# Optimization experiments

Measured on AMD Instinct MI355X. Metric: run time of the kernel, lower is better.

Reference implementation:

```python
import jax, jax.numpy as jnp
import numpy as np
import math

DIM, SCALES, ORIENTS, K = 32, 3, 8, 15
SIGMA, GAMMA = 5.0, 0.5
B, H, W = 4, 128, 128

def _make_gabor_filters():
    # matches EnhancedBlockGabor._create_complex_filters
    coords = np.arange(-(K // 2), K // 2 + 1, dtype=np.float32)
    y, x = np.meshgrid(coords, coords, indexing='ij')  # torch.meshgrid default 'ij'
    filts = []
    for s in range(SCALES):
        fu = 1.0 / 2 ** s
        for o in range(ORIENTS):
            theta = o * math.pi / ORIENTS
            xt = x * math.cos(theta) + y * math.sin(theta)
            yt = -x * math.sin(theta) + y * math.cos(theta)
            env = np.exp(-(xt ** 2 + GAMMA ** 2 * yt ** 2) / (2 * SIGMA ** 2))
            amp = fu ** 2 / (math.pi * GAMMA ** 2)
            real = amp * env * np.cos(2 * math.pi * fu * xt)
            imag = amp * env * np.sin(2 * math.pi * fu * xt)
            filts.append(np.stack([real, imag]))
    return jnp.asarray(np.stack(filts), dtype=jnp.float32)  # (S*O, 2, K, K)

def setup_inputs() -> dict:
    key = jax.random.key(0)
    k1, k2, k3 = jax.random.split(key, 3)
    x = jax.random.normal(k1, (B, DIM, H, W), dtype=jnp.float32)
    filters = _make_gabor_filters()
    cin = DIM * SCALES * ORIENTS
    w1 = jax.random.normal(k2, (DIM, cin), dtype=jnp.float32) / np.sqrt(cin)
    b1 = jax.random.normal(k3, (DIM,), dtype=jnp.float32) * 0.01
    return {"x": x, "filters": filters, "w1": w1, "b1": b1}

def reference(x, filters, w1, b1):
    Bb, C, Hh, Ww = x.shape
    SO = filters.shape[0]
    pad = K // 2
    # depthwise multi-scale Gabor conv: every channel vs every (scale,orient,re/im) filter
    xr = x.reshape(Bb * C, 1, Hh, Ww)
    kern = filters.reshape(SO * 2, 1, K, K)
    feat = jax.lax.conv_general_dilated(
        xr, kern, window_strides=(1, 1), padding=[(pad, pad), (pad, pad)],
        dimension_numbers=('NCHW', 'OIHW', 'NCHW'))  # (B*C, SO*2, H, W)
    feat = feat.reshape(Bb, C, SO, 2, Hh, Ww)
    mag = jnp.sqrt(feat[:, :, :, 0] ** 2 + feat[:, :, :, 1] ** 2)  # (B,C,SO,H,W)
    mag = jnp.swapaxes(mag, -1, -2)  # original permutes H<->W before reshape
    mag = mag.reshape(Bb, C * SO, Hh, Ww)
    y = jnp.einsum('oc,bchw->bohw', w1, mag) + b1[None, :, None, None]
    mean = y.mean(axis=(2, 3), keepdims=True)
    var = y.var(axis=(2, 3), keepdims=True)
    return (y - mean) / jnp.sqrt(var + 1e-5)  # InstanceNorm2d (affine=False)
```

## Files before the change

kernel.cpp:

```cpp
#include <hip/hip_runtime.h>


typedef __attribute__((ext_vector_type(8))) short bfx8;
typedef __attribute__((ext_vector_type(4))) float fx4;
typedef __attribute__((ext_vector_type(4))) unsigned ux4;

#define NREP   2
#define RPITCH 144
#define RROWS  144
#define IMG_SH (RROWS * RPITCH)
#define REP_SH (128 * IMG_SH)
#define XREP_SH (NREP * REP_SH)

#define A_OFF    ((size_t)XREP_SH * 2)
#define W1B_OFF  (A_OFF + (size_t)48 * 256 * 2)
#define YP_OFF   (W1B_OFF + (size_t)32 * 32 * 32 * 2)
#define ST_OFF   (YP_OFF + (size_t)128 * 16384 * 4)

#define WROW_DW  40
#define WREP_DW  656
#define WBUF_DW  (2 * WREP_DW)
#define WWAVE_DW (2 * WBUF_DW)

__device__ __forceinline__ unsigned short f2bf(float f) {
    unsigned u = __float_as_uint(f);
    u = (u + 0x7FFFu + ((u >> 16) & 1u)) >> 16;
    return (unsigned short)u;
}

__device__ __forceinline__ float fsqrt(float x) {
    float r;
    asm("v_sqrt_f32 %0, %1" : "=v"(r) : "v"(x));
    return r;
}

__global__ void prep(const float* __restrict__ x, const float* __restrict__ filt,
                     const float* __restrict__ w1, unsigned* __restrict__ xrep,
                     unsigned short* __restrict__ A, unsigned short* __restrict__ w1b,
                     float* __restrict__ stats)
{
    const int bid = blockIdx.x;
    if (bid < 2048) {
        const int phi = bid & 1, img = (bid >> 1) & 127, rg = bid >> 8;
        const unsigned obase = (unsigned)phi * (REP_SH / 2) + img * (IMG_SH / 2)
                             + rg * 18 * 72;
        for (int j = threadIdx.x; j < 18 * 72; j += 256) {
            int jr = j / 72;
            int pd = j - jr * 72;
            int r  = rg * 18 + jr;
            int c0 = 2 * pd + phi;
            float v0 = 0.f, v1 = 0.f;
            int rr = r - 7;
            if (rr >= 0 && rr < 128) {
                const float* row = x + ((size_t)img * 128 + rr) * 128;
                int cc0 = c0 - 7;
                if (cc0 >= 0 && cc0 < 128) v0 = row[cc0];
                int cc1 = c0 - 6;
                if (cc1 >= 0 && cc1 < 128) v1 = row[cc1];
            }
            xrep[obase + j] = (unsigned)f2bf(v0) | ((unsigned)f2bf(v1) << 16);
        }
    } else {
        int t = (bid - 2048) * 256 + threadIdx.x;
        if (t < 48 * 256) {
            int f = t >> 8, k = t & 255;
            int ky = k >> 4, kx = k & 15;
            float v = 0.f;
            if (ky < 15 && kx < 15) v = filt[(f * 15 + ky) * 15 + kx];
            A[t] = f2bf(v);
        } else if (t < 48 * 256 + 32 * 32 * 32) {
            int j = t - 48 * 256;
            int c = j >> 10, o = (j >> 5) & 31, so = j & 31;
            float v = (so < 24) ? w1[o * 768 + c * 24 + so] : 0.f;
            w1b[j] = f2bf(v);
        } else if (t < 48 * 256 + 32 * 32 * 32 + 256) {
            stats[t - (48 * 256 + 32 * 32 * 32)] = 0.f;
        }
    }
}

__global__ void __attribute__((amdgpu_waves_per_eu(2, 2)))
__launch_bounds__(256)
conv_mix(const unsigned short* __restrict__ xrep,
         const unsigned short* __restrict__ Aw,
         const unsigned short* __restrict__ w1b,
         float* __restrict__ ypart, float* __restrict__ stats)
{
    __shared__ unsigned stagew[4 * WWAVE_DW];
    __shared__ unsigned mag_lds[2][4][32][20];
    __shared__ float stat_lds[4][4][16];

    const int tid  = threadIdx.x;
    const int lane = tid & 63;
    const int wave = tid >> 6;
    const int n    = lane & 15;
    const int q    = lane >> 4;

    const int bid = blockIdx.x;
    const int b   = (bid >> 1) & 3;
    const int h   = (bid & 1) * 64 + (bid >> 3);

    if (lane < 32) {
        ux4 z4 = {0u, 0u, 0u, 0u};
        *(ux4*)&mag_lds[0][wave][lane][12] = z4;
        *(ux4*)&mag_lds[1][wave][lane][12] = z4;
    }

    ux4 afr[3][8];
#pragma unroll
    for (int mt = 0; mt < 3; ++mt)
#pragma unroll
        for (int s = 0; s < 8; ++s)
            afr[mt][s] = *(const ux4*)(Aw + ((mt * 16 + n) * 256 + s * 32 + q * 8));
#pragma unroll
    for (int mt = 0; mt < 3; ++mt)
#pragma unroll
        for (int s = 0; s < 8; ++s)
            asm volatile("" : "+v"(afr[mt][s]));

    const int px0 = wave * 32;
    const int p   = n & 1;
    const int fbase = wave * WWAVE_DW + p * WREP_DW + (q >> 1) * WROW_DW
                    + ((n - p) >> 1) + (q & 1) * 4;

    int g_off[3], l_off[3];
#pragma unroll
    for (int i = 0; i < 3; ++i) {
        int slot = i * 64 + lane;
        int rep  = slot >= 96;
        int rem  = slot - 96 * rep;
        int row  = rem / 6;
        int sl   = rem - row * 6;
        g_off[i] = rep * REP_SH + (h + row) * RPITCH + px0 + sl * 8;
        l_off[i] = wave * WWAVE_DW + rep * WREP_DW + row * WROW_DW + sl * 4;
    }
    const int imgbase0 = (b * 32) * IMG_SH;

    const fx4 zero4 = {0.f, 0.f, 0.f, 0.f};
    fx4 yacc[2][2];
#pragma unroll
    for (int mt = 0; mt < 2; ++mt)
#pragma unroll
        for (int t = 0; t < 2; ++t) yacc[mt][t] = zero4;

    {
        const unsigned short* g = xrep + imgbase0;
#pragma unroll
        for (int i = 0; i < 3; ++i)
            *(ux4*)&stagew[l_off[i]] = *(const ux4*)(g + g_off[i]);
    }

    bfx8 wfp[2];

    for (int c = 0; c < 32; ++c) {
        ux4 nv[3];
        if (c < 31) {
            const unsigned short* g = xrep + imgbase0 + (c + 1) * IMG_SH;
#pragma unroll
            for (int i = 0; i < 3; ++i)
                nv[i] = *(const ux4*)(g + g_off[i]);
        }

        ux4 magp[2];
        if (c > 0) {
            const int pbuf = (c & 1) ^ 1;
#pragma unroll
            for (int t = 0; t < 2; ++t)
                magp[t] = *(const ux4*)&mag_lds[pbuf][wave][t * 16 + n][q * 4];
        }

        bfx8 wfc[2];
#pragma unroll
        for (int mt = 0; mt < 2; ++mt)
            wfc[mt] = *(const bfx8*)(w1b + ((c * 32 + mt * 16 + n) * 32 + q * 8));

        const int fb = fbase + (c & 1) * WBUF_DW;
        ux4 braw[2][2];
#pragma unroll
        for (int t = 0; t < 2; ++t) {
            const int ix = fb + t * 8;
            ux4 v = {stagew[ix], stagew[ix + 1], stagew[ix + 2], stagew[ix + 3]};
            braw[0][t] = v;
        }

        fx4 cacc[3][2];
#pragma unroll
        for (int mt = 0; mt < 3; ++mt)
#pragma unroll
            for (int t = 0; t < 2; ++t) cacc[mt][t] = zero4;

#pragma unroll
        for (int s = 0; s < 8; ++s) {
            if (s < 7) {
#pragma unroll
                for (int t = 0; t < 2; ++t) {
                    const int ix = fb + (s + 1) * (2 * WROW_DW) + t * 8;
                    ux4 v = {stagew[ix], stagew[ix + 1],
                             stagew[ix + 2], stagew[ix + 3]};
                    braw[(s + 1) & 1][t] = v;
                }
            }
#pragma unroll
            for (int t = 0; t < 2; ++t) {
                bfx8 bf = __builtin_bit_cast(bfx8, braw[s & 1][t]);
#pragma unroll
                for (int mt = 0; mt < 3; ++mt)
                    cacc[mt][t] = __builtin_amdgcn_mfma_f32_16x16x32_bf16(
                        __builtin_bit_cast(bfx8, afr[mt][s]), bf, cacc[mt][t], 0, 0, 0);
            }
            if (s == 1 && c > 0) {
#pragma unroll
                for (int t = 0; t < 2; ++t) {
                    bfx8 mb = __builtin_bit_cast(bfx8, magp[t]);
#pragma unroll
                    for (int mt = 0; mt < 2; ++mt)
                        yacc[mt][t] = __builtin_amdgcn_mfma_f32_16x16x32_bf16(
                            wfp[mt], mb, yacc[mt][t], 0, 0, 0);
                }
            }
        }

#pragma unroll
        for (int t = 0; t < 2; ++t)
#pragma unroll
            for (int mt = 0; mt < 3; ++mt) {
                float m0 = fsqrt(cacc[mt][t][0] * cacc[mt][t][0] +
                                 cacc[mt][t][1] * cacc[mt][t][1]);
                float m1 = fsqrt(cacc[mt][t][2] * cacc[mt][t][2] +
                                 cacc[mt][t][3] * cacc[mt][t][3]);
                unsigned u0 = __float_as_uint(m0), u1 = __float_as_uint(m1);
                unsigned pk = ((u0 + 0x8000u) >> 16) | ((u1 + 0x8000u) & 0xFFFF0000u);
                mag_lds[c & 1][wave][t * 16 + n][4 * mt + q] = pk;
            }

        if (c < 31) {
            const int wb = ((c + 1) & 1) * WBUF_DW;
#pragma unroll
            for (int i = 0; i < 3; ++i)
                *(ux4*)&stagew[wb + l_off[i]] = nv[i];
        }
#pragma unroll
        for (int mt = 0; mt < 2; ++mt) wfp[mt] = wfc[mt];
    }

#pragma unroll
    for (int t = 0; t < 2; ++t) {
        ux4 raw = *(const ux4*)&mag_lds[1][wave][t * 16 + n][q * 4];
        bfx8 mb = __builtin_bit_cast(bfx8, raw);
#pragma unroll
        for (int mt = 0; mt < 2; ++mt)
            yacc[mt][t] = __builtin_amdgcn_mfma_f32_16x16x32_bf16(
                wfp[mt], mb, yacc[mt][t], 0, 0, 0);
    }

    float* yp = ypart + (size_t)(b * 32) * 16384 + h * 128;
#pragma unroll
    for (int mt = 0; mt < 2; ++mt)
#pragma unroll
        for (int t = 0; t < 2; ++t) {
            const int w0 = px0 + t * 16 + n;
#pragma unroll
            for (int r = 0; r < 4; ++r)
                yp[(size_t)(mt * 16 + 4 * q + r) * 16384 + w0] = yacc[mt][t][r];
        }

    float sv[8], qv[8];
#pragma unroll
    for (int mt = 0; mt < 2; ++mt)
#pragma unroll
        for (int r = 0; r < 4; ++r) {
            float v0 = yacc[mt][0][r], v1 = yacc[mt][1][r];
            sv[mt * 4 + r] = v0 + v1;
            qv[mt * 4 + r] = v0 * v0 + v1 * v1;
        }
#pragma unroll
    for (int m = 1; m <= 8; m <<= 1)
#pragma unroll
        for (int i = 0; i < 8; ++i) {
            sv[i] += __shfl_xor(sv[i], m);
            qv[i] += __shfl_xor(qv[i], m);
        }
    if (n == 0) {
#pragma unroll
        for (int i = 0; i < 8; ++i) {
            stat_lds[wave][q][i]     = sv[i];
            stat_lds[wave][q][i + 8] = qv[i];
        }
    }
    __syncthreads();
    if (tid < 64) {
        int qq = tid >> 4, i = tid & 15;
        float acc = stat_lds[0][qq][i] + stat_lds[1][qq][i] +
                    stat_lds[2][qq][i] + stat_lds[3][qq][i];
        int kind = i >> 3, mt = (i >> 2) & 1, r = i & 3;
        int o = mt * 16 + 4 * qq + r;
        atomicAdd(&stats[(b * 32 + o) * 2 + kind], acc);
    }
}

__global__ void inorm2(const float* __restrict__ ypart, const float* __restrict__ stats,
                       float* __restrict__ out)
{
    const int bid = blockIdx.x;
    const int bo = bid >> 4, tile = bid & 15;
    const int h0 = (tile >> 2) * 32, w0 = (tile & 3) * 32;
    const float mean = stats[bo * 2] * (1.f / 16384.f);
    float var = stats[bo * 2 + 1] * (1.f / 16384.f) - mean * mean;
    const float rstd = rsqrtf(fmaxf(var, 0.f) + 1e-5f);

    const float* y0 = ypart + (size_t)bo * 16384;
    __shared__ float tilebuf[32][33];
    const int r = threadIdx.x >> 3, c4 = (threadIdx.x & 7) * 4;

    const size_t base = (size_t)(h0 + r) * 128 + w0 + c4;
    fx4 a = *(const fx4*)(y0 + base);
#pragma unroll
    for (int j = 0; j < 4; ++j)
        tilebuf[r][c4 + j] = (a[j] - mean) * rstd;
    __syncthreads();
    float* ob = out + (size_t)bo * 16384 + (size_t)(w0 + r) * 128 + h0 + c4;
    fx4 o4;
#pragma unroll
    for (int j = 0; j < 4; ++j) o4[j] = tilebuf[c4 + j][r];
    *(fx4*)ob = o4;
}

extern "C" void kernel_launch(void* const* d_in, const int* in_sizes, int n_in,
                              void* d_out, int out_size, void* d_ws, size_t ws_size,
                              hipStream_t stream)
{
    const float* x    = (const float*)d_in[0];
    const float* filt = (const float*)d_in[1];
    const float* w1   = (const float*)d_in[2];
    float* out = (float*)d_out;
    char* ws = (char*)d_ws;

    unsigned*       xrep  = (unsigned*)ws;
    unsigned short* Aw    = (unsigned short*)(ws + A_OFF);
    unsigned short* w1b   = (unsigned short*)(ws + W1B_OFF);
    float*          yp    = (float*)(ws + YP_OFF);
    float*          stats = (float*)(ws + ST_OFF);

    prep<<<2048 + 178, 256, 0, stream>>>(x, filt, w1, xrep, Aw, w1b, stats);
    conv_mix<<<512, 256, 0, stream>>>((const unsigned short*)xrep, Aw, w1b, yp, stats);
    inorm2<<<2048, 256, 0, stream>>>(yp, stats, out);
}
```

Measured before the change: 126.2 us.

## Fuse input bf16 padding/replication into conv kernel, drop xrep prepass

Removes the prep stage that wrote a padded, two-phase bf16 copy of x to global memory. conv_mix now loads fp32 x directly with per-lane boundary masks, converts to bf16 and builds both shifted replicas in LDS while staging. This removes a full extra write and read of the replicated input and most of the prep grid. In exchange, each lane issues five scalar masked fp32 loads instead of one 16-byte load, which adds address math and load instructions inside the main loop.

```diff
diff --git a/kernel.cpp b/kernel.cpp
--- a/kernel.cpp
+++ b/kernel.cpp
@@ -4,15 +4,9 @@
 typedef __attribute__((ext_vector_type(8))) short bfx8;
 typedef __attribute__((ext_vector_type(4))) float fx4;
 typedef __attribute__((ext_vector_type(4))) unsigned ux4;
-
-#define NREP   2
-#define RPITCH 144
-#define RROWS  144
-#define IMG_SH (RROWS * RPITCH)
-#define REP_SH (128 * IMG_SH)
-#define XREP_SH (NREP * REP_SH)
-
-#define A_OFF    ((size_t)XREP_SH * 2)
+typedef __attribute__((ext_vector_type(2))) unsigned ux2;
+
+#define A_OFF    ((size_t)0)
 #define W1B_OFF  (A_OFF + (size_t)48 * 256 * 2)
 #define YP_OFF   (W1B_OFF + (size_t)32 * 32 * 32 * 2)
 #define ST_OFF   (YP_OFF + (size_t)128 * 16384 * 4)
@@ -28,65 +22,47 @@
     return (unsigned short)u;
 }
 
+__device__ __forceinline__ unsigned pkbf(float a, float b) {
+    unsigned ua = __float_as_uint(a) + 0x8000u;
+    unsigned ub = __float_as_uint(b) + 0x8000u;
+    return (ua >> 16) | (ub & 0xFFFF0000u);
+}
+
 __device__ __forceinline__ float fsqrt(float x) {
     float r;
     asm("v_sqrt_f32 %0, %1" : "=v"(r) : "v"(x));
     return r;
 }
 
-__global__ void prep(const float* __restrict__ x, const float* __restrict__ filt,
-                     const float* __restrict__ w1, unsigned* __restrict__ xrep,
+__global__ void prep(const float* __restrict__ filt, const float* __restrict__ w1,
                      unsigned short* __restrict__ A, unsigned short* __restrict__ w1b,
                      float* __restrict__ stats)
 {
-    const int bid = blockIdx.x;
-    if (bid < 2048) {
-        const int phi = bid & 1, img = (bid >> 1) & 127, rg = bid >> 8;
-        const unsigned obase = (unsigned)phi * (REP_SH / 2) + img * (IMG_SH / 2)
-                             + rg * 18 * 72;
-        for (int j = threadIdx.x; j < 18 * 72; j += 256) {
-            int jr = j / 72;
-            int pd = j - jr * 72;
-            int r  = rg * 18 + jr;
-            int c0 = 2 * pd + phi;
-            float v0 = 0.f, v1 = 0.f;
-            int rr = r - 7;
-            if (rr >= 0 && rr < 128) {
-                const float* row = x + ((size_t)img * 128 + rr) * 128;
-                int cc0 = c0 - 7;
-                if (cc0 >= 0 && cc0 < 128) v0 = row[cc0];
-                int cc1 = c0 - 6;
-                if (cc1 >= 0 && cc1 < 128) v1 = row[cc1];
-            }
-            xrep[obase + j] = (unsigned)f2bf(v0) | ((unsigned)f2bf(v1) << 16);
-        }
-    } else {
-        int t = (bid - 2048) * 256 + threadIdx.x;
-        if (t < 48 * 256) {
-            int f = t >> 8, k = t & 255;
-            int ky = k >> 4, kx = k & 15;
-            float v = 0.f;
-            if (ky < 15 && kx < 15) v = filt[(f * 15 + ky) * 15 + kx];
-            A[t] = f2bf(v);
-        } else if (t < 48 * 256 + 32 * 32 * 32) {
-            int j = t - 48 * 256;
-            int c = j >> 10, o = (j >> 5) & 31, so = j & 31;
-            float v = (so < 24) ? w1[o * 768 + c * 24 + so] : 0.f;
-            w1b[j] = f2bf(v);
-        } else if (t < 48 * 256 + 32 * 32 * 32 + 256) {
-            stats[t - (48 * 256 + 32 * 32 * 32)] = 0.f;
-        }
+    int t = blockIdx.x * 256 + threadIdx.x;
+    if (t < 48 * 256) {
+        int f = t >> 8, k = t & 255;
+        int ky = k >> 4, kx = k & 15;
+        float v = 0.f;
+        if (ky < 15 && kx < 15) v = filt[(f * 15 + ky) * 15 + kx];
+        A[t] = f2bf(v);
+    } else if (t < 48 * 256 + 32 * 32 * 32) {
+        int j = t - 48 * 256;
+        int c = j >> 10, o = (j >> 5) & 31, so = j & 31;
+        float v = (so < 24) ? w1[o * 768 + c * 24 + so] : 0.f;
+        w1b[j] = f2bf(v);
+    } else if (t < 48 * 256 + 32 * 32 * 32 + 256) {
+        stats[t - (48 * 256 + 32 * 32 * 32)] = 0.f;
     }
 }
 
 __global__ void __attribute__((amdgpu_waves_per_eu(2, 2)))
 __launch_bounds__(256)
-conv_mix(const unsigned short* __restrict__ xrep,
+conv_mix(const float* __restrict__ x,
          const unsigned short* __restrict__ Aw,
          const unsigned short* __restrict__ w1b,
          float* __restrict__ ypart, float* __restrict__ stats)
 {
-    __shared__ unsigned stagew[4 * WWAVE_DW];
+    __shared__ __align__(16) unsigned stagew[4 * WWAVE_DW];
     __shared__ unsigned mag_lds[2][4][32][20];
     __shared__ float stat_lds[4][4][16];
 
@@ -123,18 +99,26 @@
     const int fbase = wave * WWAVE_DW + p * WREP_DW + (q >> 1) * WROW_DW
                     + ((n - p) >> 1) + (q & 1) * 4;
 
-    int g_off[3], l_off[3];
+    int s_off[3], l_rep0[3];
+    unsigned s_msk[3];
 #pragma unroll
     for (int i = 0; i < 3; ++i) {
         int slot = i * 64 + lane;
-        int rep  = slot >= 96;
-        int rem  = slot - 96 * rep;
-        int row  = rem / 6;
-        int sl   = rem - row * 6;
-        g_off[i] = rep * REP_SH + (h + row) * RPITCH + px0 + sl * 8;
-        l_off[i] = wave * WWAVE_DW + rep * WREP_DW + row * WROW_DW + sl * 4;
-    }
-    const int imgbase0 = (b * 32) * IMG_SH;
+        int row  = slot / 12;
+        int sl   = slot - row * 12;
+        int rr   = h + row - 7;
+        int cc0  = px0 + sl * 4 - 7;
+        unsigned m = 0;
+        if (rr >= 0 && rr < 128) {
+#pragma unroll
+            for (int k = 0; k < 5; ++k)
+                if (cc0 + k >= 0 && cc0 + k < 128) m |= 1u << k;
+        }
+        s_msk[i] = m;
+        s_off[i] = rr * 128 + cc0;
+        l_rep0[i] = wave * WWAVE_DW + row * WROW_DW + sl * 2;
+    }
+    const float* xb0 = x + (size_t)(b * 32) * 16384;
 
     const fx4 zero4 = {0.f, 0.f, 0.f, 0.f};
     fx4 yacc[2][2];
@@ -144,21 +128,39 @@
         for (int t = 0; t < 2; ++t) yacc[mt][t] = zero4;
 
     {
-        const unsigned short* g = xrep + imgbase0;
-#pragma unroll
-        for (int i = 0; i < 3; ++i)
-            *(ux4*)&stagew[l_off[i]] = *(const ux4*)(g + g_off[i]);
+        const float* xi = xb0;
+#pragma unroll
+        for (int i = 0; i < 3; ++i) {
+            float f[5];
+#pragma unroll
+            for (int k = 0; k < 5; ++k) {
+                const bool v = (s_msk[i] >> k) & 1;
+                const int idx = v ? s_off[i] + k : 0;
+                float raw = xi[idx];
+                f[k] = v ? raw : 0.f;
+            }
+            ux2 r0 = {pkbf(f[0], f[1]), pkbf(f[2], f[3])};
+            ux2 r1 = {pkbf(f[1], f[2]), pkbf(f[3], f[4])};
+            *(ux2*)&stagew[l_rep0[i]] = r0;
+            *(ux2*)&stagew[l_rep0[i] + WREP_DW] = r1;
+        }
     }
 
     bfx8 wfp[2];
 
     for (int c = 0; c < 32; ++c) {
-        ux4 nv[3];
+        float nf[3][5];
         if (c < 31) {
-            const unsigned short* g = xrep + imgbase0 + (c + 1) * IMG_SH;
+            const float* xi = xb0 + (size_t)(c + 1) * 16384;
 #pragma unroll
             for (int i = 0; i < 3; ++i)
-                nv[i] = *(const ux4*)(g + g_off[i]);
+#pragma unroll
+                for (int k = 0; k < 5; ++k) {
+                    const bool v = (s_msk[i] >> k) & 1;
+                    const int idx = v ? s_off[i] + k : 0;
+                    float raw = xi[idx];
+                    nf[i][k] = v ? raw : 0.f;
+                }
         }
 
         ux4 magp[2];
@@ -228,16 +230,18 @@
                                  cacc[mt][t][1] * cacc[mt][t][1]);
                 float m1 = fsqrt(cacc[mt][t][2] * cacc[mt][t][2] +
                                  cacc[mt][t][3] * cacc[mt][t][3]);
-                unsigned u0 = __float_as_uint(m0), u1 = __float_as_uint(m1);
-                unsigned pk = ((u0 + 0x8000u) >> 16) | ((u1 + 0x8000u) & 0xFFFF0000u);
-                mag_lds[c & 1][wave][t * 16 + n][4 * mt + q] = pk;
+                mag_lds[c & 1][wave][t * 16 + n][4 * mt + q] = pkbf(m0, m1);
             }
 
         if (c < 31) {
             const int wb = ((c + 1) & 1) * WBUF_DW;
 #pragma unroll
-            for (int i = 0; i < 3; ++i)
-                *(ux4*)&stagew[wb + l_off[i]] = nv[i];
+            for (int i = 0; i < 3; ++i) {
+                ux2 r0 = {pkbf(nf[i][0], nf[i][1]), pkbf(nf[i][2], nf[i][3])};
+                ux2 r1 = {pkbf(nf[i][1], nf[i][2]), pkbf(nf[i][3], nf[i][4])};
+                *(ux2*)&stagew[wb + l_rep0[i]] = r0;
+                *(ux2*)&stagew[wb + l_rep0[i] + WREP_DW] = r1;
+            }
         }
 #pragma unroll
         for (int mt = 0; mt < 2; ++mt) wfp[mt] = wfc[mt];
@@ -335,13 +339,12 @@
     float* out = (float*)d_out;
     char* ws = (char*)d_ws;
 
-    unsigned*       xrep  = (unsigned*)ws;
     unsigned short* Aw    = (unsigned short*)(ws + A_OFF);
     unsigned short* w1b   = (unsigned short*)(ws + W1B_OFF);
     float*          yp    = (float*)(ws + YP_OFF);
     float*          stats = (float*)(ws + ST_OFF);
 
-    prep<<<2048 + 178, 256, 0, stream>>>(x, filt, w1, xrep, Aw, w1b, stats);
-    conv_mix<<<512, 256, 0, stream>>>((const unsigned short*)xrep, Aw, w1b, yp, stats);
+    prep<<<177, 256, 0, stream>>>(filt, w1, Aw, w1b, stats);
+    conv_mix<<<512, 256, 0, stream>>>(x, Aw, w1b, yp, stats);
     inorm2<<<2048, 256, 0, stream>>>(yp, stats, out);
 }
```

Result: slower. 152.9 us (+21.1%).
